# Kernel tuning notes

Measured on AMD Instinct MI355X. Metric: run time of the kernel, lower is better.

Reference implementation:

```python
import jax, jax.numpy as jnp
import numpy as np

N = 8192
D = 384


def setup_inputs() -> dict:
    key = jax.random.key(0)
    kx, kq, kk, kv, kf = jax.random.split(key, 5)
    x = jax.random.normal(kx, (N, D), dtype=jnp.float32)
    Wq = jax.random.uniform(kq, (D, D), dtype=jnp.float32)
    Wk = jax.random.uniform(kk, (D, D), dtype=jnp.float32)
    Wv = jax.random.uniform(kv, (D, D), dtype=jnp.float32)
    ffws = jax.random.uniform(kf, (D,), dtype=jnp.float32)
    return {"x": x, "Wq": Wq, "Wk": Wk, "Wv": Wv, "ffws": ffws}


def reference(x, Wq, Wk, Wv, ffws):
    def layer(h):
        # Q = Wq @ h.T -> Q.T = h @ Wq.T ; scores = Q.T @ K = (h Wq.T)(Wk h.T)
        Qt = h @ Wq.T                    # [N, D]
        K = Wk @ h.T                     # [D, N]
        scores = jax.nn.softmax(Qt @ K, axis=1)  # [N, N], torch implicit dim=1
        Vt = h @ Wv.T                    # [N, D]
        # weighted_sum double-loop == scores @ Vt (soft_sim is square so
        # choice(size()) always returns N)
        return scores @ Vt               # [N, D]

    z = layer(layer(x))
    # o = sigmoid(sum(ffws * z[-1]))
    return jax.nn.sigmoid(jnp.sum(ffws * z[-1]))
```

## Files before the change

### kernel.cpp

```cpp
#include <hip/hip_runtime.h>
#include <hip/hip_bf16.h>
#include <math.h>

static constexpr int kN = 8192;
static constexpr int kD = 384;
static constexpr int kND = kN * kD;

typedef __attribute__((ext_vector_type(8))) short short8;
typedef __attribute__((ext_vector_type(4))) float f32x4;

__device__ __forceinline__ ushort f2bf(float f) {
  union { float f; unsigned int i; } cv; cv.f = f;
  unsigned int lsb = (cv.i >> 16) & 1u;
  unsigned int r = cv.i + 0x7fffu + lsb;
  return (ushort)(r >> 16);
}
__device__ __forceinline__ float bf2f(ushort u) {
  union { unsigned int i; float f; } cv; cv.i = ((unsigned int)u) << 16;
  return cv.f;
}
__device__ __forceinline__ f32x4 mfma_bf16(short8 a, short8 b, f32x4 c) {
  return __builtin_amdgcn_mfma_f32_16x16x32_bf16(a, b, c, 0, 0, 0);
}
__device__ __forceinline__ void bar_lds() {
  asm volatile("s_waitcnt lgkmcnt(0)" ::: "memory");
  __builtin_amdgcn_s_barrier();
}

__global__ __launch_bounds__(512) void proj_mfma(
    const float* __restrict__ x, const float* __restrict__ Wq,
    const float* __restrict__ Wk, const float* __restrict__ Wv,
    ushort* __restrict__ Qh, ushort* __restrict__ Kh,
    ushort* __restrict__ VTh)
{
  __shared__ ushort XH[128 * 32], XL[128 * 32];
  __shared__ ushort WH[96 * 32], WL[96 * 32];

  const int tid = threadIdx.x;
  const int w = tid >> 6;
  const int lane = tid & 63;
  const int l15 = lane & 15;
  const int hi4 = lane >> 4;
  const int i0 = blockIdx.x * 128;
  const int j0 = blockIdx.y * 96;
  const int m = blockIdx.z;
  const float* W = (m == 0) ? Wq : (m == 1) ? Wk : Wv;

  const f32x4 zf = {0.f, 0.f, 0.f, 0.f};
  f32x4 acc[6];
#pragma unroll
  for (int ct = 0; ct < 6; ++ct) acc[ct] = zf;

  const int xrow = tid >> 2;
  const int xc8 = (tid & 3) * 8;

  for (int dc = 0; dc < 12; ++dc) {
    const int d0 = dc * 32;
    {
      const float* src = x + (size_t)(i0 + xrow) * kD + d0 + xc8;
      const float4 v0 = *reinterpret_cast<const float4*>(src);
      const float4 v1 = *reinterpret_cast<const float4*>(src + 4);
      const float vs[8] = {v0.x, v0.y, v0.z, v0.w, v1.x, v1.y, v1.z, v1.w};
      ushort hh[8], ll[8];
#pragma unroll
      for (int j = 0; j < 8; ++j) {
        const ushort h = f2bf(vs[j]);
        hh[j] = h;
        ll[j] = f2bf(vs[j] - bf2f(h));
      }
      *reinterpret_cast<uint4*>(&XH[xrow * 32 + xc8]) =
          *reinterpret_cast<const uint4*>(hh);
      *reinterpret_cast<uint4*>(&XL[xrow * 32 + xc8]) =
          *reinterpret_cast<const uint4*>(ll);
    }
    if (tid < 384) {
      const float* src = W + (size_t)(j0 + xrow) * kD + d0 + xc8;
      const float4 v0 = *reinterpret_cast<const float4*>(src);
      const float4 v1 = *reinterpret_cast<const float4*>(src + 4);
      const float vs[8] = {v0.x, v0.y, v0.z, v0.w, v1.x, v1.y, v1.z, v1.w};
      ushort hh[8], ll[8];
#pragma unroll
      for (int j = 0; j < 8; ++j) {
        const ushort h = f2bf(vs[j]);
        hh[j] = h;
        ll[j] = f2bf(vs[j] - bf2f(h));
      }
      *reinterpret_cast<uint4*>(&WH[xrow * 32 + xc8]) =
          *reinterpret_cast<const uint4*>(hh);
      *reinterpret_cast<uint4*>(&WL[xrow * 32 + xc8]) =
          *reinterpret_cast<const uint4*>(ll);
    }
    __syncthreads();
    const short8 xa = *reinterpret_cast<const short8*>(
        &XH[(16 * w + l15) * 32 + 8 * hi4]);
    const short8 xb = *reinterpret_cast<const short8*>(
        &XL[(16 * w + l15) * 32 + 8 * hi4]);
#pragma unroll
    for (int ct = 0; ct < 6; ++ct) {
      const short8 wh = *reinterpret_cast<const short8*>(
          &WH[(16 * ct + l15) * 32 + 8 * hi4]);
      const short8 wl = *reinterpret_cast<const short8*>(
          &WL[(16 * ct + l15) * 32 + 8 * hi4]);
      acc[ct] = mfma_bf16(xa, wh, acc[ct]);
      acc[ct] = mfma_bf16(xa, wl, acc[ct]);
      acc[ct] = mfma_bf16(xb, wh, acc[ct]);
    }
    __syncthreads();
  }

  if (m < 2) {
    ushort* Y = (m == 0) ? Qh : Kh;
#pragma unroll
    for (int ct = 0; ct < 6; ++ct)
#pragma unroll
      for (int r = 0; r < 4; ++r)
        Y[(size_t)(i0 + 16 * w + 4 * hi4 + r) * kD + j0 + 16 * ct + l15] =
            f2bf(acc[ct][r]);
  } else {
#pragma unroll
    for (int ct = 0; ct < 6; ++ct) {
      ushort4 h;
      ushort* hp = &h.x;
#pragma unroll
      for (int r = 0; r < 4; ++r) hp[r] = f2bf(acc[ct][r]);
      *reinterpret_cast<ushort4*>(
          &VTh[(size_t)(j0 + 16 * ct + l15) * kN + i0 + 16 * w + 4 * hi4]) = h;
    }
  }
}

static constexpr int SPLITf = 4;
static constexpr int KEYSf = kN / SPLITf;
static constexpr int NTIL = KEYSf / 128;

static constexpr int OFF_QH = 0;
static constexpr int OFF_P  = 50176;

__global__ __launch_bounds__(512, 2) void flash_mfma(
    const ushort* __restrict__ Qh,
    const ushort* __restrict__ Kh,
    const ushort* __restrict__ VTh,
    float* __restrict__ Opart, float* __restrict__ ml)
{
  __shared__ ushort LDSU[67584];
  __shared__ float MLB[2048];

  const int tid = threadIdx.x;
  const int w = tid >> 6;
  const int lane = tid & 63;
  const int l15 = lane & 15;
  const int hi4 = lane >> 4;
  const int sp = blockIdx.x;
  const int i0 = blockIdx.y * 128;
  const int kg0 = sp * KEYSf;

  {
    const int row = tid >> 2;
    const int sg = (tid & 3) * 96;
    const ushort* sh = Qh + (size_t)(i0 + row) * kD + sg;
    ushort* dh = LDSU + OFF_QH + row * 392 + sg;
#pragma unroll
    for (int u = 0; u < 12; ++u)
      *reinterpret_cast<uint4*>(dh + 8 * u) =
          *reinterpret_cast<const uint4*>(sh + 8 * u);
  }

  const f32x4 zf = {0.f, 0.f, 0.f, 0.f};
  f32x4 o[8][3];
#pragma unroll
  for (int qt = 0; qt < 8; ++qt)
#pragma unroll
    for (int c = 0; c < 3; ++c) o[qt][c] = zf;
  float m_run[8], l_run[8];
#pragma unroll
  for (int qt = 0; qt < 8; ++qt) { m_run[qt] = -INFINITY; l_run[qt] = 0.f; }

  __syncthreads();

  for (int kb = 0; kb < NTIL; ++kb) {
    const int kg = kg0 + kb * 128;

    f32x4 sacc[8];
#pragma unroll
    for (int qt = 0; qt < 8; ++qt) sacc[qt] = zf;
    const size_t kbase = (size_t)(kg + 16 * w + l15) * kD + 8 * hi4;
    short8 ka[12];
#pragma unroll
    for (int ks = 0; ks < 12; ++ks)
      ka[ks] = *reinterpret_cast<const short8*>(Kh + kbase + 32 * ks);
    __builtin_amdgcn_sched_barrier(0);
#pragma unroll
    for (int ks = 0; ks < 12; ++ks) {
      const int d0 = 32 * ks;
#pragma unroll
      for (int qt = 0; qt < 8; ++qt) {
        const short8 qh = *reinterpret_cast<const short8*>(
            LDSU + OFF_QH + (16 * qt + l15) * 392 + d0 + 8 * hi4);
        sacc[qt] = mfma_bf16(ka[ks], qh, sacc[qt]);
      }
    }

    float mt8[8];
#pragma unroll
    for (int qt = 0; qt < 8; ++qt) {
      float mt = fmaxf(fmaxf(sacc[qt][0], sacc[qt][1]),
                       fmaxf(sacc[qt][2], sacc[qt][3]));
      mt = fmaxf(mt, __shfl_xor(mt, 16, 64));
      mt = fmaxf(mt, __shfl_xor(mt, 32, 64));
      mt8[qt] = mt;
    }
    if (lane < 16) {
#pragma unroll
      for (int qt = 0; qt < 8; ++qt) MLB[w * 128 + qt * 16 + l15] = mt8[qt];
    }
    bar_lds();
    float sc[8];
#pragma unroll
    for (int qt = 0; qt < 8; ++qt) {
      float Mt = MLB[qt * 16 + l15];
#pragma unroll
      for (int w2 = 1; w2 < 8; ++w2)
        Mt = fmaxf(Mt, MLB[w2 * 128 + qt * 16 + l15]);
      const float mnew = fmaxf(m_run[qt], Mt);
      sc[qt] = __expf(m_run[qt] - mnew);
      m_run[qt] = mnew;
      const float p0 = __expf(sacc[qt][0] - mnew);
      const float p1 = __expf(sacc[qt][1] - mnew);
      const float p2 = __expf(sacc[qt][2] - mnew);
      const float p3 = __expf(sacc[qt][3] - mnew);
      float ls = (p0 + p1) + (p2 + p3);
      ls += __shfl_xor(ls, 16, 64);
      ls += __shfl_xor(ls, 32, 64);
      if (lane < 16) MLB[1024 + w * 128 + qt * 16 + l15] = ls;
      uint2 HH;
      HH.x = (unsigned int)f2bf(p0) | ((unsigned int)f2bf(p1) << 16);
      HH.y = (unsigned int)f2bf(p2) | ((unsigned int)f2bf(p3) << 16);
      const int pi = (16 * qt + l15) * 136 + 16 * w + 4 * hi4;
      *reinterpret_cast<uint2*>(LDSU + OFF_P + pi) = HH;
#pragma unroll
      for (int r = 0; r < 4; ++r) {
        const float scr_ = __shfl(sc[qt], 4 * hi4 + r, 64);
#pragma unroll
        for (int c = 0; c < 3; ++c) o[qt][c][r] *= scr_;
      }
    }
    bar_lds();
#pragma unroll
    for (int qt = 0; qt < 8; ++qt) {
      float acc = MLB[1024 + qt * 16 + l15];
#pragma unroll
      for (int w2 = 1; w2 < 8; ++w2)
        acc += MLB[1024 + w2 * 128 + qt * 16 + l15];
      l_run[qt] = l_run[qt] * sc[qt] + acc;
    }

    short8 vv[12];
#pragma unroll
    for (int c = 0; c < 3; ++c)
#pragma unroll
      for (int kv = 0; kv < 4; ++kv)
        vv[c * 4 + kv] = *reinterpret_cast<const short8*>(
            VTh + (size_t)(48 * w + 16 * c + l15) * kN + kg + 32 * kv + 8 * hi4);
    __builtin_amdgcn_sched_barrier(0);
#pragma unroll
    for (int kv = 0; kv < 4; ++kv) {
      short8 pf[8];
#pragma unroll
      for (int qt = 0; qt < 8; ++qt)
        pf[qt] = *reinterpret_cast<const short8*>(
            LDSU + OFF_P + (16 * qt + l15) * 136 + 32 * kv + 8 * hi4);
#pragma unroll
      for (int c = 0; c < 3; ++c) {
#pragma unroll
        for (int qt = 0; qt < 8; ++qt)
          o[qt][c] = mfma_bf16(pf[qt], vv[c * 4 + kv], o[qt][c]);
      }
    }
  }

#pragma unroll
  for (int qt = 0; qt < 8; ++qt)
#pragma unroll
    for (int c = 0; c < 3; ++c)
#pragma unroll
      for (int r = 0; r < 4; ++r)
        Opart[(size_t)sp * kND + (i0 + 16 * qt + 4 * hi4 + r) * kD +
              48 * w + 16 * c + l15] = o[qt][c][r];
  if (w == 0 && lane < 16) {
#pragma unroll
    for (int qt = 0; qt < 8; ++qt) {
      const int mi = (sp * kN + i0 + 16 * qt + l15) * 2;
      ml[mi] = m_run[qt];
      ml[mi + 1] = l_run[qt];
    }
  }
}

__global__ __launch_bounds__(256) void merge_kernel(
    const float* __restrict__ Opart, const float* __restrict__ ml,
    float* __restrict__ O)
{
  const size_t idx = (size_t)blockIdx.x * 256 + threadIdx.x;
  const size_t i = idx / kD;
  float m = ml[i * 2];
#pragma unroll
  for (int sp = 1; sp < SPLITf; ++sp)
    m = fmaxf(m, ml[((size_t)sp * kN + i) * 2]);
  float den = 0.f, acc = 0.f;
#pragma unroll
  for (int sp = 0; sp < SPLITf; ++sp) {
    const float e = __expf(ml[((size_t)sp * kN + i) * 2] - m);
    den += e * ml[((size_t)sp * kN + i) * 2 + 1];
    acc += e * Opart[(size_t)sp * kND + idx];
  }
  O[idx] = acc / den;
}

__global__ __launch_bounds__(64) void qrow_kernel(
    const float* __restrict__ h1, const float* __restrict__ Wq,
    float* __restrict__ q2)
{
  const int j = blockIdx.x;
  const int lane = threadIdx.x;
  const float* hr = h1 + (size_t)(kN - 1) * kD;
  float acc = 0.f;
  for (int d = lane; d < kD; d += 64) acc += hr[d] * Wq[(size_t)j * kD + d];
#pragma unroll
  for (int off = 32; off > 0; off >>= 1) acc += __shfl_xor(acc, off, 64);
  if (lane == 0) q2[j] = acc;
}

__global__ __launch_bounds__(384) void u_kernel(
    const float* __restrict__ Wk, const float* __restrict__ q2,
    float* __restrict__ u)
{
  __shared__ float qs[kD];
  const int d = threadIdx.x;
  qs[d] = q2[d];
  __syncthreads();
  float acc = 0.f;
  for (int k = 0; k < kD; ++k) acc += Wk[(size_t)k * kD + d] * qs[k];
  u[d] = acc;
}

__global__ __launch_bounds__(256) void logits_kernel(
    const float* __restrict__ h1, const float* __restrict__ u,
    float* __restrict__ lg)
{
  const int wave = threadIdx.x >> 6;
  const int lane = threadIdx.x & 63;
  const int j = blockIdx.x * 4 + wave;
  float acc = 0.f;
#pragma unroll
  for (int t = 0; t < kD / 64; ++t) {
    const int d = lane + t * 64;
    acc += h1[(size_t)j * kD + d] * u[d];
  }
#pragma unroll
  for (int off = 32; off > 0; off >>= 1) acc += __shfl_xor(acc, off, 64);
  if (lane == 0) lg[j] = acc;
}

__global__ __launch_bounds__(1024) void smax_kernel(
    const float* __restrict__ lg, float* __restrict__ wgt)
{
  __shared__ float red[16];
  const int t = threadIdx.x;
  const int wave = t >> 6;
  const int lane = t & 63;
  float v[8];
  float mx = -INFINITY;
#pragma unroll
  for (int s = 0; s < 8; ++s) {
    v[s] = lg[t + 1024 * s];
    mx = fmaxf(mx, v[s]);
  }
#pragma unroll
  for (int off = 32; off > 0; off >>= 1) mx = fmaxf(mx, __shfl_xor(mx, off, 64));
  if (lane == 0) red[wave] = mx;
  __syncthreads();
  if (t == 0) {
    float m = red[0];
    for (int i = 1; i < 16; ++i) m = fmaxf(m, red[i]);
    red[0] = m;
  }
  __syncthreads();
  const float m = red[0];
  __syncthreads();
  float sum = 0.f;
#pragma unroll
  for (int s = 0; s < 8; ++s) {
    v[s] = expf(v[s] - m);
    sum += v[s];
  }
#pragma unroll
  for (int off = 32; off > 0; off >>= 1) sum += __shfl_xor(sum, off, 64);
  if (lane == 0) red[wave] = sum;
  __syncthreads();
  if (t == 0) {
    float S = 0.f;
    for (int i = 0; i < 16; ++i) S += red[i];
    red[0] = S;
  }
  __syncthreads();
  const float invS = 1.0f / red[0];
#pragma unroll
  for (int s = 0; s < 8; ++s) wgt[t + 1024 * s] = v[s] * invS;
}

__global__ __launch_bounds__(384) void wsum_kernel(
    const float* __restrict__ wgt, const float* __restrict__ h1,
    float* __restrict__ part)
{
  __shared__ float wl[256];
  const int b = blockIdx.x;
  const int t = threadIdx.x;
  if (t < 256) wl[t] = wgt[b * 256 + t];
  __syncthreads();
  const float* Hp = h1 + (size_t)b * 256 * kD;
  float acc = 0.f;
  for (int j = 0; j < 256; ++j) acc += wl[j] * Hp[(size_t)j * kD + t];
  part[b * kD + t] = acc;
}

__global__ __launch_bounds__(384) void final2_kernel(
    const float* __restrict__ part, const float* __restrict__ Wv,
    const float* __restrict__ ffws, float* __restrict__ out)
{
  __shared__ float zs[kD];
  __shared__ float red[6];
  const int t = threadIdx.x;
  const int wave = t >> 6;
  const int lane = t & 63;
  float z = 0.f;
#pragma unroll
  for (int b = 0; b < 32; ++b) z += part[b * kD + t];
  zs[t] = z;
  __syncthreads();
  float zv = 0.f;
  for (int k = 0; k < kD; ++k) zv += Wv[(size_t)t * kD + k] * zs[k];
  float val = zv * ffws[t];
#pragma unroll
  for (int off = 32; off > 0; off >>= 1) val += __shfl_xor(val, off, 64);
  if (lane == 0) red[wave] = val;
  __syncthreads();
  if (t == 0) {
    float s = red[0];
    for (int i = 1; i < 6; ++i) s += red[i];
    out[0] = 1.0f / (1.0f + expf(-s));
  }
}

extern "C" void kernel_launch(void* const* d_in, const int* in_sizes, int n_in,
                              void* d_out, int out_size, void* d_ws, size_t ws_size,
                              hipStream_t stream) {
  const float* x    = (const float*)d_in[0];
  const float* Wq   = (const float*)d_in[1];
  const float* Wk   = (const float*)d_in[2];
  const float* Wv   = (const float*)d_in[3];
  const float* ffws = (const float*)d_in[4];
  float* out = (float*)d_out;
  char* wsb = (char*)d_ws;

  ushort* Qh  = (ushort*)wsb;
  ushort* Kh  = Qh + kND;
  ushort* VTh = Kh + kND;
  const size_t bfQKV = 3 * (size_t)kND * 2;
  float* Opart = (float*)(wsb + bfQKV);
  float* ml    = Opart + (size_t)SPLITf * kND;
  float* h1    = ml + (size_t)SPLITf * kN * 2;
  float* q2    = h1 + (size_t)kND;
  float* u     = q2 + kD;
  float* lg    = u + kD;
  float* wgt   = lg + kN;
  float* part  = wgt + kN;

  proj_mfma<<<dim3(kN / 128, kD / 96, 3), 512, 0, stream>>>(
      x, Wq, Wk, Wv, Qh, Kh, VTh);
  flash_mfma<<<dim3(SPLITf, kN / 128), 512, 0, stream>>>(
      Qh, Kh, VTh, Opart, ml);
  merge_kernel<<<(kN * kD) / 256, 256, 0, stream>>>(Opart, ml, h1);
  qrow_kernel<<<kD, 64, 0, stream>>>(h1, Wq, q2);
  u_kernel<<<1, 384, 0, stream>>>(Wk, q2, u);
  logits_kernel<<<kN / 4, 256, 0, stream>>>(h1, u, lg);
  smax_kernel<<<1, 1024, 0, stream>>>(lg, wgt);
  wsum_kernel<<<32, 384, 0, stream>>>(wgt, h1, part);
  final2_kernel<<<1, 384, 0, stream>>>(part, Wv, ffws, out);
}
```

Baseline: 286.2 us.

## Fuse QKV projections per block, store bf16 normalized partials, hoist V loads

```diff
diff --git a/kernel.cpp b/kernel.cpp
--- a/kernel.cpp
+++ b/kernel.cpp
@@ -34,7 +34,7 @@
     ushort* __restrict__ VTh)
 {
   __shared__ ushort XH[128 * 32], XL[128 * 32];
-  __shared__ ushort WH[96 * 32], WL[96 * 32];
+  __shared__ ushort WH[3][96 * 32], WL[3][96 * 32];
 
   const int tid = threadIdx.x;
   const int w = tid >> 6;
@@ -43,13 +43,14 @@
   const int hi4 = lane >> 4;
   const int i0 = blockIdx.x * 128;
   const int j0 = blockIdx.y * 96;
-  const int m = blockIdx.z;
-  const float* W = (m == 0) ? Wq : (m == 1) ? Wk : Wv;
+  const float* Wm[3] = {Wq, Wk, Wv};
 
   const f32x4 zf = {0.f, 0.f, 0.f, 0.f};
-  f32x4 acc[6];
-#pragma unroll
-  for (int ct = 0; ct < 6; ++ct) acc[ct] = zf;
+  f32x4 acc[3][6];
+#pragma unroll
+  for (int m = 0; m < 3; ++m)
+#pragma unroll
+    for (int ct = 0; ct < 6; ++ct) acc[m][ct] = zf;
 
   const int xrow = tid >> 2;
   const int xc8 = (tid & 3) * 8;
@@ -74,21 +75,24 @@
           *reinterpret_cast<const uint4*>(ll);
     }
     if (tid < 384) {
-      const float* src = W + (size_t)(j0 + xrow) * kD + d0 + xc8;
-      const float4 v0 = *reinterpret_cast<const float4*>(src);
-      const float4 v1 = *reinterpret_cast<const float4*>(src + 4);
-      const float vs[8] = {v0.x, v0.y, v0.z, v0.w, v1.x, v1.y, v1.z, v1.w};
-      ushort hh[8], ll[8];
-#pragma unroll
-      for (int j = 0; j < 8; ++j) {
-        const ushort h = f2bf(vs[j]);
-        hh[j] = h;
-        ll[j] = f2bf(vs[j] - bf2f(h));
+#pragma unroll
+      for (int m = 0; m < 3; ++m) {
+        const float* src = Wm[m] + (size_t)(j0 + xrow) * kD + d0 + xc8;
+        const float4 v0 = *reinterpret_cast<const float4*>(src);
+        const float4 v1 = *reinterpret_cast<const float4*>(src + 4);
+        const float vs[8] = {v0.x, v0.y, v0.z, v0.w, v1.x, v1.y, v1.z, v1.w};
+        ushort hh[8], ll[8];
+#pragma unroll
+        for (int j = 0; j < 8; ++j) {
+          const ushort h = f2bf(vs[j]);
+          hh[j] = h;
+          ll[j] = f2bf(vs[j] - bf2f(h));
+        }
+        *reinterpret_cast<uint4*>(&WH[m][xrow * 32 + xc8]) =
+            *reinterpret_cast<const uint4*>(hh);
+        *reinterpret_cast<uint4*>(&WL[m][xrow * 32 + xc8]) =
+            *reinterpret_cast<const uint4*>(ll);
       }
-      *reinterpret_cast<uint4*>(&WH[xrow * 32 + xc8]) =
-          *reinterpret_cast<const uint4*>(hh);
-      *reinterpret_cast<uint4*>(&WL[xrow * 32 + xc8]) =
-          *reinterpret_cast<const uint4*>(ll);
     }
     __syncthreads();
     const short8 xa = *reinterpret_cast<const short8*>(
@@ -96,36 +100,38 @@
     const short8 xb = *reinterpret_cast<const short8*>(
         &XL[(16 * w + l15) * 32 + 8 * hi4]);
 #pragma unroll
-    for (int ct = 0; ct < 6; ++ct) {
-      const short8 wh = *reinterpret_cast<const short8*>(
-          &WH[(16 * ct + l15) * 32 + 8 * hi4]);
-      const short8 wl = *reinterpret_cast<const short8*>(
-          &WL[(16 * ct + l15) * 32 + 8 * hi4]);
-      acc[ct] = mfma_bf16(xa, wh, acc[ct]);
-      acc[ct] = mfma_bf16(xa, wl, acc[ct]);
-      acc[ct] = mfma_bf16(xb, wh, acc[ct]);
+    for (int m = 0; m < 3; ++m) {
+#pragma unroll
+      for (int ct = 0; ct < 6; ++ct) {
+        const short8 wh = *reinterpret_cast<const short8*>(
+            &WH[m][(16 * ct + l15) * 32 + 8 * hi4]);
+        const short8 wl = *reinterpret_cast<const short8*>(
+            &WL[m][(16 * ct + l15) * 32 + 8 * hi4]);
+        acc[m][ct] = mfma_bf16(xa, wh, acc[m][ct]);
+        acc[m][ct] = mfma_bf16(xa, wl, acc[m][ct]);
+        acc[m][ct] = mfma_bf16(xb, wh, acc[m][ct]);
+      }
     }
     __syncthreads();
   }
 
-  if (m < 2) {
-    ushort* Y = (m == 0) ? Qh : Kh;
-#pragma unroll
-    for (int ct = 0; ct < 6; ++ct)
-#pragma unroll
-      for (int r = 0; r < 4; ++r)
-        Y[(size_t)(i0 + 16 * w + 4 * hi4 + r) * kD + j0 + 16 * ct + l15] =
-            f2bf(acc[ct][r]);
-  } else {
-#pragma unroll
-    for (int ct = 0; ct < 6; ++ct) {
-      ushort4 h;
-      ushort* hp = &h.x;
-#pragma unroll
-      for (int r = 0; r < 4; ++r) hp[r] = f2bf(acc[ct][r]);
-      *reinterpret_cast<ushort4*>(
-          &VTh[(size_t)(j0 + 16 * ct + l15) * kN + i0 + 16 * w + 4 * hi4]) = h;
-    }
+#pragma unroll
+  for (int ct = 0; ct < 6; ++ct)
+#pragma unroll
+    for (int r = 0; r < 4; ++r) {
+      const size_t oi =
+          (size_t)(i0 + 16 * w + 4 * hi4 + r) * kD + j0 + 16 * ct + l15;
+      Qh[oi] = f2bf(acc[0][ct][r]);
+      Kh[oi] = f2bf(acc[1][ct][r]);
+    }
+#pragma unroll
+  for (int ct = 0; ct < 6; ++ct) {
+    ushort4 h;
+    ushort* hp = &h.x;
+#pragma unroll
+    for (int r = 0; r < 4; ++r) hp[r] = f2bf(acc[2][ct][r]);
+    *reinterpret_cast<ushort4*>(
+        &VTh[(size_t)(j0 + 16 * ct + l15) * kN + i0 + 16 * w + 4 * hi4]) = h;
   }
 }
 
@@ -140,7 +146,7 @@
     const ushort* __restrict__ Qh,
     const ushort* __restrict__ Kh,
     const ushort* __restrict__ VTh,
-    float* __restrict__ Opart, float* __restrict__ ml)
+    ushort* __restrict__ Opart, float* __restrict__ ml)
 {
   __shared__ ushort LDSU[67584];
   __shared__ float MLB[2048];
@@ -200,27 +206,34 @@
       }
     }
 
-    float mt8[8];
 #pragma unroll
     for (int qt = 0; qt < 8; ++qt) {
       float mt = fmaxf(fmaxf(sacc[qt][0], sacc[qt][1]),
                        fmaxf(sacc[qt][2], sacc[qt][3]));
       mt = fmaxf(mt, __shfl_xor(mt, 16, 64));
       mt = fmaxf(mt, __shfl_xor(mt, 32, 64));
-      mt8[qt] = mt;
-    }
-    if (lane < 16) {
-#pragma unroll
-      for (int qt = 0; qt < 8; ++qt) MLB[w * 128 + qt * 16 + l15] = mt8[qt];
+      if (lane < 16) MLB[(qt * 16 + l15) * 8 + w] = mt;
     }
     bar_lds();
+
+    short8 vv[12];
+#pragma unroll
+    for (int c = 0; c < 3; ++c)
+#pragma unroll
+      for (int kv = 0; kv < 4; ++kv)
+        vv[c * 4 + kv] = *reinterpret_cast<const short8*>(
+            VTh + (size_t)(48 * w + 16 * c + l15) * kN + kg + 32 * kv + 8 * hi4);
+    __builtin_amdgcn_sched_barrier(0);
+
     float sc[8];
 #pragma unroll
     for (int qt = 0; qt < 8; ++qt) {
-      float Mt = MLB[qt * 16 + l15];
-#pragma unroll
-      for (int w2 = 1; w2 < 8; ++w2)
-        Mt = fmaxf(Mt, MLB[w2 * 128 + qt * 16 + l15]);
+      const float4 ma =
+          *reinterpret_cast<const float4*>(&MLB[(qt * 16 + l15) * 8]);
+      const float4 mb =
+          *reinterpret_cast<const float4*>(&MLB[(qt * 16 + l15) * 8 + 4]);
+      const float Mt = fmaxf(fmaxf(fmaxf(ma.x, ma.y), fmaxf(ma.z, ma.w)),
+                             fmaxf(fmaxf(mb.x, mb.y), fmaxf(mb.z, mb.w)));
       const float mnew = fmaxf(m_run[qt], Mt);
       sc[qt] = __expf(m_run[qt] - mnew);
       m_run[qt] = mnew;
@@ -231,7 +244,7 @@
       float ls = (p0 + p1) + (p2 + p3);
       ls += __shfl_xor(ls, 16, 64);
       ls += __shfl_xor(ls, 32, 64);
-      if (lane < 16) MLB[1024 + w * 128 + qt * 16 + l15] = ls;
+      if (lane < 16) MLB[1024 + (qt * 16 + l15) * 8 + w] = ls;
       uint2 HH;
       HH.x = (unsigned int)f2bf(p0) | ((unsigned int)f2bf(p1) << 16);
       HH.y = (unsigned int)f2bf(p2) | ((unsigned int)f2bf(p3) << 16);
@@ -247,21 +260,15 @@
     bar_lds();
 #pragma unroll
     for (int qt = 0; qt < 8; ++qt) {
-      float acc = MLB[1024 + qt * 16 + l15];
-#pragma unroll
-      for (int w2 = 1; w2 < 8; ++w2)
-        acc += MLB[1024 + w2 * 128 + qt * 16 + l15];
-      l_run[qt] = l_run[qt] * sc[qt] + acc;
-    }
-
-    short8 vv[12];
-#pragma unroll
-    for (int c = 0; c < 3; ++c)
-#pragma unroll
-      for (int kv = 0; kv < 4; ++kv)
-        vv[c * 4 + kv] = *reinterpret_cast<const short8*>(
-            VTh + (size_t)(48 * w + 16 * c + l15) * kN + kg + 32 * kv + 8 * hi4);
-    __builtin_amdgcn_sched_barrier(0);
+      const float4 la =
+          *reinterpret_cast<const float4*>(&MLB[1024 + (qt * 16 + l15) * 8]);
+      const float4 lb =
+          *reinterpret_cast<const float4*>(&MLB[1024 + (qt * 16 + l15) * 8 + 4]);
+      const float ls = ((la.x + la.y) + (la.z + la.w)) +
+                       ((lb.x + lb.y) + (lb.z + lb.w));
+      l_run[qt] = l_run[qt] * sc[qt] + ls;
+    }
+
 #pragma unroll
     for (int kv = 0; kv < 4; ++kv) {
       short8 pf[8];
@@ -279,13 +286,17 @@
   }
 
 #pragma unroll
-  for (int qt = 0; qt < 8; ++qt)
-#pragma unroll
-    for (int c = 0; c < 3; ++c)
-#pragma unroll
-      for (int r = 0; r < 4; ++r)
+  for (int qt = 0; qt < 8; ++qt) {
+    const float linv = 1.0f / l_run[qt];
+#pragma unroll
+    for (int r = 0; r < 4; ++r) {
+      const float lr = __shfl(linv, 4 * hi4 + r, 64);
+#pragma unroll
+      for (int c = 0; c < 3; ++c)
         Opart[(size_t)sp * kND + (i0 + 16 * qt + 4 * hi4 + r) * kD +
-              48 * w + 16 * c + l15] = o[qt][c][r];
+              48 * w + 16 * c + l15] = f2bf(o[qt][c][r] * lr);
+    }
+  }
   if (w == 0 && lane < 16) {
 #pragma unroll
     for (int qt = 0; qt < 8; ++qt) {
@@ -297,7 +308,7 @@
 }
 
 __global__ __launch_bounds__(256) void merge_kernel(
-    const float* __restrict__ Opart, const float* __restrict__ ml,
+    const ushort* __restrict__ Opart, const float* __restrict__ ml,
     float* __restrict__ O)
 {
   const size_t idx = (size_t)blockIdx.x * 256 + threadIdx.x;
@@ -309,9 +320,10 @@
   float den = 0.f, acc = 0.f;
 #pragma unroll
   for (int sp = 0; sp < SPLITf; ++sp) {
-    const float e = __expf(ml[((size_t)sp * kN + i) * 2] - m);
-    den += e * ml[((size_t)sp * kN + i) * 2 + 1];
-    acc += e * Opart[(size_t)sp * kND + idx];
+    const float e = __expf(ml[((size_t)sp * kN + i) * 2] - m) *
+                    ml[((size_t)sp * kN + i) * 2 + 1];
+    den += e;
+    acc += e * bf2f(Opart[(size_t)sp * kND + idx]);
   }
   O[idx] = acc / den;
 }
@@ -465,9 +477,8 @@
   ushort* Qh  = (ushort*)wsb;
   ushort* Kh  = Qh + kND;
   ushort* VTh = Kh + kND;
-  const size_t bfQKV = 3 * (size_t)kND * 2;
-  float* Opart = (float*)(wsb + bfQKV);
-  float* ml    = Opart + (size_t)SPLITf * kND;
+  ushort* Opart = VTh + kND;
+  float* ml    = (float*)(Opart + (size_t)SPLITf * kND);
   float* h1    = ml + (size_t)SPLITf * kN * 2;
   float* q2    = h1 + (size_t)kND;
   float* u     = q2 + kD;
@@ -475,7 +486,7 @@
   float* wgt   = lg + kN;
   float* part  = wgt + kN;
 
-  proj_mfma<<<dim3(kN / 128, kD / 96, 3), 512, 0, stream>>>(
+  proj_mfma<<<dim3(kN / 128, kD / 96), 512, 0, stream>>>(
       x, Wq, Wk, Wv, Qh, Kh, VTh);
   flash_mfma<<<dim3(SPLITf, kN / 128), 512, 0, stream>>>(
       Qh, Kh, VTh, Opart, ml);
```

New measurement: 284.8 us. About the same (-0.5%).
